# Kernel tuning notes

Hardware: AMD Instinct MI355X
Metric: run time of the kernel (lower is better)

Reference implementation:

```python
import math
import jax, jax.numpy as jnp
import numpy as np

B, T, E = 4, 2048, 768
H, D = 3, E // 3  # 3 heads, head_dim = emb_sz // 3
USE_MASK = True


def setup_inputs() -> dict:
    key = jax.random.key(0)
    ks = jax.random.split(key, 8)
    s_in = 1.0 / math.sqrt(E)
    return {
        "inputs_for_keys": jax.random.normal(ks[0], (B, T, E), jnp.float32),
        "inputs_for_values": jax.random.normal(ks[1], (B, T, E), jnp.float32),
        "inputs_for_queries": jax.random.normal(ks[2], (B, T, E), jnp.float32),
        # per-head projection weights, stacked over head axis: [H, E, D]
        "Wk": jax.random.normal(ks[3], (H, E, D), jnp.float32) * s_in,
        "Wq": jax.random.normal(ks[4], (H, E, D), jnp.float32) * s_in,
        "Wv": jax.random.normal(ks[5], (H, E, D), jnp.float32) * s_in,
        # final Dense(emb_sz)
        "Wo": jax.random.normal(ks[6], (E, E), jnp.float32) * s_in,
        "bo": jnp.zeros((E,), jnp.float32),
    }


def reference(inputs_for_keys, inputs_for_values, inputs_for_queries, Wk, Wq, Wv, Wo, bo):
    # Project per head: [B,T,E] x [H,E,D] -> [B,H,T,D]
    K = jnp.einsum('bte,hed->bhtd', inputs_for_keys, Wk)
    V = jnp.einsum('bte,hed->bhtd', inputs_for_values, Wv)
    Q = jnp.einsum('bte,hed->bhtd', inputs_for_queries, Wq)
    # NOTE: original scales by sqrt(window_size_keys) = sqrt(T), not sqrt(D)
    scores = jnp.einsum('bhqd,bhkd->bhqk', Q, K) / math.sqrt(T)
    if USE_MASK:
        mask = jnp.triu(jnp.full((T, T), -jnp.inf, dtype=scores.dtype), k=1)
        scores = scores + mask
    attn = jax.nn.softmax(scores, axis=-1)  # [B,H,Tq,Tk]
    z = jnp.einsum('bhqk,bhkd->bhqd', attn, V)  # [B,H,T,D]
    # concat heads in order head1,head2,head3 along last axis -> [B,T,E]
    z = jnp.transpose(z, (0, 2, 1, 3)).reshape(B, T, H * D)
    return z @ Wo + bo
```

## Files before the change

### kernel.cpp

```cpp
#include <hip/hip_runtime.h>
#include <hip/hip_bf16.h>
#include <math.h>

#define B_ 4
#define T_ 2048
#define E_ 768
#define H_ 3
#define D_ 256
#define LOG2E 1.4426950408889634f

typedef __attribute__((ext_vector_type(8))) _Float16 half8;
typedef __attribute__((ext_vector_type(8))) unsigned short ushort8;
typedef __attribute__((ext_vector_type(4))) float f32x4;

static __device__ inline unsigned short f2h(float x) {
    _Float16 h = (_Float16)x;
    return *reinterpret_cast<unsigned short*>(&h);
}

#define GLOAD_LDS(SRC, DST) \
    __builtin_amdgcn_global_load_lds( \
        (const __attribute__((address_space(1))) void*)(SRC), \
        (__attribute__((address_space(3))) void*)(DST), 16, 0, 0)

__global__ __launch_bounds__(256)
void transpose_cast_all(const float* __restrict__ Wk, const float* __restrict__ Wq,
                        const float* __restrict__ Wv, const float* __restrict__ Wo,
                        unsigned short* __restrict__ WTk, unsigned short* __restrict__ WTq,
                        unsigned short* __restrict__ WTv, unsigned short* __restrict__ WoT)
{
    __shared__ float tile[32][33];
    const int z = blockIdx.z;
    const float* in; unsigned short* out; int R, C;
    if (z < 9) {
        const int mat = z / 3, hd = z % 3;
        R = E_; C = D_;
        in  = (mat == 0 ? Wk  : mat == 1 ? Wq  : Wv)  + (long)hd * E_ * D_;
        out = (mat == 0 ? WTk : mat == 1 ? WTq : WTv) + (long)hd * D_ * E_;
    } else {
        R = E_; C = E_;
        in = Wo; out = WoT;
    }
    const int c0 = blockIdx.x * 32;
    const int r0 = blockIdx.y * 32;
    if (c0 >= C) return;
    const int t  = threadIdx.x;
    const int cc = t & 31, rr = t >> 5;
    #pragma unroll
    for (int i = 0; i < 4; ++i)
        tile[rr + i * 8][cc] = in[(long)(r0 + rr + i * 8) * C + c0 + cc];
    __syncthreads();
    const int rr2 = t & 31, cc2 = t >> 5;
    #pragma unroll
    for (int i = 0; i < 4; ++i)
        out[(long)(c0 + cc2 + i * 8) * R + r0 + rr2] = f2h(tile[rr2][cc2 + i * 8]);
}

template<bool CONVA, bool OUT16, bool TRANSC>
__device__ __forceinline__
void gemm_body(const float* Af, const unsigned short* Ah, const unsigned short* Bz,
               void* Cz, const float* bias, int K, int lda, int ldc,
               int m0, int n0, int tid)
{
    __shared__ unsigned short As[128 * 32];
    __shared__ unsigned short Bs[128 * 32];

    const int lane = tid & 63, wid = tid >> 6;
    const int wm = wid >> 1, wn = wid & 1;
    const int fr = lane & 15, fg = lane >> 4;

    f32x4 acc[4][4];
    #pragma unroll
    for (int mt = 0; mt < 4; ++mt)
        #pragma unroll
        for (int nt = 0; nt < 4; ++nt) acc[mt][nt] = (f32x4)(0.f);

    for (int k0 = 0; k0 < K; k0 += 32) {
        #pragma unroll
        for (int i = 0; i < 2; ++i) {
            const int G = tid + i * 256;
            const int row = G >> 2, g = G & 3;
            ushort8 pa;
            if (CONVA) {
                const float* s = Af + (long)(m0 + row) * lda + k0 + g * 8;
                float4 f0 = *(const float4*)s, f1 = *(const float4*)(s + 4);
                pa[0] = f2h(f0.x); pa[1] = f2h(f0.y); pa[2] = f2h(f0.z); pa[3] = f2h(f0.w);
                pa[4] = f2h(f1.x); pa[5] = f2h(f1.y); pa[6] = f2h(f1.z); pa[7] = f2h(f1.w);
            } else {
                pa = *(const ushort8*)(Ah + (long)(m0 + row) * lda + k0 + g * 8);
            }
            *(ushort8*)&As[row * 32 + g * 8] = pa;
            *(ushort8*)&Bs[row * 32 + g * 8] =
                *(const ushort8*)(Bz + (long)(n0 + row) * K + k0 + g * 8);
        }
        __syncthreads();

        half8 a[4], b[4];
        #pragma unroll
        for (int mt = 0; mt < 4; ++mt)
            a[mt] = *(const half8*)&As[(wm * 64 + mt * 16 + fr) * 32 + fg * 8];
        #pragma unroll
        for (int nt = 0; nt < 4; ++nt)
            b[nt] = *(const half8*)&Bs[(wn * 64 + nt * 16 + fr) * 32 + fg * 8];
        #pragma unroll
        for (int mt = 0; mt < 4; ++mt)
            #pragma unroll
            for (int nt = 0; nt < 4; ++nt)
                acc[mt][nt] = __builtin_amdgcn_mfma_f32_16x16x32_f16(
                                  a[mt], b[nt], acc[mt][nt], 0, 0, 0);
        __syncthreads();
    }

    #pragma unroll
    for (int nt = 0; nt < 4; ++nt) {
        const int col = n0 + wn * 64 + nt * 16 + fr;
        const float badd = bias ? bias[col] : 0.f;
        #pragma unroll
        for (int mt = 0; mt < 4; ++mt) {
            const int row = m0 + wm * 64 + mt * 16 + fg * 4;
            #pragma unroll
            for (int reg = 0; reg < 4; ++reg) {
                const float vv = acc[mt][nt][reg] + badd;
                if (TRANSC)
                    ((unsigned short*)Cz)[(long)col * ldc + row + reg] = f2h(vv);
                else if (OUT16)
                    ((unsigned short*)Cz)[(long)(row + reg) * ldc + col] = f2h(vv);
                else
                    ((float*)Cz)[(long)(row + reg) * ldc + col] = vv;
            }
        }
    }
}

template<bool CONVA, bool OUT16>
__global__ __launch_bounds__(256)
void gemm_mfma(const void* __restrict__ Av, const unsigned short* __restrict__ Bt,
               void* __restrict__ Cv, const float* __restrict__ bias,
               int K, int Hdiv, int lda, int ldc, long sA, long sB, long sC)
{
    const int z = blockIdx.z;
    const float*          Af = (const float*)Av          + (long)(z / Hdiv) * sA;
    const unsigned short* Ah = (const unsigned short*)Av + (long)(z / Hdiv) * sA;
    const unsigned short* Bz = Bt + (long)(z % Hdiv) * sB;
    void* Cz = OUT16 ? (void*)((unsigned short*)Cv + (long)z * sC)
                     : (void*)((float*)Cv + (long)z * sC);
    gemm_body<CONVA, OUT16, false>(Af, Ah, Bz, Cz, bias, K, lda, ldc,
                                   blockIdx.y * 128, blockIdx.x * 128, threadIdx.x);
}

__global__ __launch_bounds__(256)
void qkv_proj(const float* __restrict__ Xk, const float* __restrict__ Xv,
              const float* __restrict__ Xq,
              const unsigned short* __restrict__ WTk, const unsigned short* __restrict__ WTv,
              const unsigned short* __restrict__ WTq,
              unsigned short* __restrict__ Kp, unsigned short* __restrict__ Vt,
              unsigned short* __restrict__ Qp)
{
    const int z = blockIdx.z;
    const int which = z / 12, bh = z % 12;
    const int b = bh / H_, h = bh % H_;
    const int m0 = blockIdx.y * 128, n0 = blockIdx.x * 128;
    const int tid = threadIdx.x;
    if (which == 1) {
        const float* Af = Xv + (long)b * T_ * E_;
        const unsigned short* Bz = WTv + (long)h * D_ * E_;
        unsigned short* Cz = Vt + (long)bh * D_ * T_;
        gemm_body<true, true, true>(Af, nullptr, Bz, Cz, nullptr, E_, E_, T_, m0, n0, tid);
    } else {
        const float* X = (which == 0) ? Xk : Xq;
        const unsigned short* W = (which == 0) ? WTk : WTq;
        unsigned short* P = (which == 0) ? Kp : Qp;
        const float* Af = X + (long)b * T_ * E_;
        const unsigned short* Bz = W + (long)h * D_ * E_;
        unsigned short* Cz = P + (long)bh * T_ * D_;
        gemm_body<true, true, false>(Af, nullptr, Bz, Cz, nullptr, E_, E_, D_, m0, n0, tid);
    }
}

__global__ __launch_bounds__(512, 1)
void flash_lds(const unsigned short* __restrict__ Qb, const unsigned short* __restrict__ Kb,
               const unsigned short* __restrict__ Vtb, unsigned short* __restrict__ Z2h,
               float scale_log2e)
{
    __shared__ unsigned short Ktile[2][64 * 256];
    __shared__ unsigned short Vtile[2][256 * 64];
    __shared__ unsigned short Ps[8][16 * 72];

    const int p  = blockIdx.x;
    const int l  = (p & 7) * 24 + (p >> 3);
    const int bh = l >> 4;
    const int pi = l & 15;
    const int b = bh / H_, h = bh % H_;
    const int tid = threadIdx.x;
    const int w = tid >> 6, lane = tid & 63;
    const int g = lane >> 4, fr = lane & 15;
    const int qw0 = (w < 4) ? (pi * 64 + w * 16) : ((31 - pi) * 64 + (w - 4) * 16);

    const unsigned short* kg = Kb  + (long)bh * T_ * D_;
    const unsigned short* vg = Vtb + (long)bh * D_ * T_;

    const unsigned short* qrow = Qb + ((long)bh * T_ + qw0 + fr) * D_;
    const _Float16 hs = (_Float16)scale_log2e;
    half8 qf[8];
    #pragma unroll
    for (int c = 0; c < 8; ++c) {
        qf[c] = *(const half8*)(qrow + c * 32 + g * 8);
        qf[c] *= hs;
    }

    f32x4 o[16];
    #pragma unroll
    for (int dt = 0; dt < 16; ++dt) o[dt] = (f32x4)(0.f);
    float mrow[4] = {-INFINITY, -INFINITY, -INFINITY, -INFINITY};
    float lrow[4] = {0.f, 0.f, 0.f, 0.f};

    const int nkt = 32 - pi;

    auto STAGE = [&](int bufi, int kt) {
        const int k0 = kt * 64;
        #pragma unroll
        for (int i = 0; i < 4; ++i) {
            const int L = tid + i * 512;
            const int r = L >> 5, cg = L & 31;
            GLOAD_LDS(kg + (long)(k0 + r) * D_ + ((cg ^ (r & 7)) * 8),
                      &Ktile[bufi][L * 8]);
        }
        #pragma unroll
        for (int i = 0; i < 4; ++i) {
            const int L = tid + i * 512;
            const int dr = L >> 3, gq = L & 7;
            GLOAD_LDS(vg + (long)dr * T_ + k0 + ((gq ^ (dr & 7)) * 8),
                      &Vtile[bufi][L * 8]);
        }
    };

    STAGE(0, 0);
    int buf = 0;
    for (int kt = 0; kt < nkt; ++kt) {
        asm volatile("s_waitcnt vmcnt(0)" ::: "memory");
        __builtin_amdgcn_sched_barrier(0);
        __builtin_amdgcn_s_barrier();
        __builtin_amdgcn_sched_barrier(0);
        if (kt + 1 < nkt)
            STAGE(buf ^ 1, kt + 1);

        const int k0 = kt * 64;
        if (k0 <= qw0 + 15) {
            f32x4 s[4];
            #pragma unroll
            for (int nt = 0; nt < 4; ++nt) s[nt] = (f32x4)(0.f);
            const int kkey = fr & 7;
            __builtin_amdgcn_s_setprio(1);
            #pragma unroll
            for (int c = 0; c < 8; ++c) {
                #pragma unroll
                for (int nt = 0; nt < 4; ++nt) {
                    const int kr = nt * 16 + fr;
                    half8 kf = *(const half8*)&Ktile[buf][(kr * 32 + ((c * 4 + g) ^ kkey)) * 8];
                    s[nt] = __builtin_amdgcn_mfma_f32_16x16x32_f16(qf[c], kf, s[nt], 0, 0, 0);
                }
            }
            __builtin_amdgcn_s_setprio(0);

            const bool diag = (k0 + 63 > qw0);
            float sv[4][4];
            #pragma unroll
            for (int nt = 0; nt < 4; ++nt)
                #pragma unroll
                for (int reg = 0; reg < 4; ++reg) {
                    float v = s[nt][reg];
                    if (diag && (k0 + nt * 16 + fr > qw0 + g * 4 + reg)) v = -INFINITY;
                    sv[nt][reg] = v;
                }

            float pmax[4];
            #pragma unroll
            for (int reg = 0; reg < 4; ++reg)
                pmax[reg] = fmaxf(fmaxf(sv[0][reg], sv[1][reg]),
                                  fmaxf(sv[2][reg], sv[3][reg]));
            const bool ok = (pmax[0] <= mrow[0] + 8.f) && (pmax[1] <= mrow[1] + 8.f)
                         && (pmax[2] <= mrow[2] + 8.f) && (pmax[3] <= mrow[3] + 8.f);
            if (!__all(ok)) {
                #pragma unroll
                for (int reg = 0; reg < 4; ++reg) {
                    float tm = pmax[reg];
                    tm = fmaxf(tm, __shfl_xor(tm, 1));
                    tm = fmaxf(tm, __shfl_xor(tm, 2));
                    tm = fmaxf(tm, __shfl_xor(tm, 4));
                    tm = fmaxf(tm, __shfl_xor(tm, 8));
                    const float mnew = fmaxf(mrow[reg], tm);
                    const float alpha = exp2f(mrow[reg] - mnew);
                    mrow[reg] = mnew;
                    lrow[reg] *= alpha;
                    #pragma unroll
                    for (int dt = 0; dt < 16; ++dt) o[dt][reg] *= alpha;
                }
            }
            #pragma unroll
            for (int nt = 0; nt < 4; ++nt)
                #pragma unroll
                for (int reg = 0; reg < 4; ++reg) {
                    const float pp = exp2f(sv[nt][reg] - mrow[reg]);
                    lrow[reg] += pp;
                    Ps[w][(g * 4 + reg) * 72 + nt * 16 + fr] = f2h(pp);
                }

            const half8 pf0 = *(const half8*)&Ps[w][fr * 72 + g * 8];
            const half8 pf1 = *(const half8*)&Ps[w][fr * 72 + 32 + g * 8];

            __builtin_amdgcn_s_setprio(1);
            #pragma unroll
            for (int dt = 0; dt < 16; ++dt) {
                const int dr = dt * 16 + fr;
                const int key = dr & 7;
                half8 vf0 = *(const half8*)&Vtile[buf][(dr * 8 + (g ^ key)) * 8];
                o[dt] = __builtin_amdgcn_mfma_f32_16x16x32_f16(pf0, vf0, o[dt], 0, 0, 0);
                half8 vf1 = *(const half8*)&Vtile[buf][(dr * 8 + ((g + 4) ^ key)) * 8];
                o[dt] = __builtin_amdgcn_mfma_f32_16x16x32_f16(pf1, vf1, o[dt], 0, 0, 0);
            }
            __builtin_amdgcn_s_setprio(0);
        }
        buf ^= 1;
    }

    float inv[4];
    #pragma unroll
    for (int reg = 0; reg < 4; ++reg) {
        float ps = lrow[reg];
        ps += __shfl_xor(ps, 1);
        ps += __shfl_xor(ps, 2);
        ps += __shfl_xor(ps, 4);
        ps += __shfl_xor(ps, 8);
        inv[reg] = 1.f / ps;
    }
    const long rowbase = ((long)b * T_ + qw0 + g * 4) * E_ + h * D_;
    #pragma unroll
    for (int reg = 0; reg < 4; ++reg) {
        unsigned short* dst = Z2h + rowbase + (long)reg * E_ + fr;
        #pragma unroll
        for (int dt = 0; dt < 16; ++dt)
            dst[dt * 16] = f2h(o[dt][reg] * inv[reg]);
    }
}

extern "C" void kernel_launch(void* const* d_in, const int* in_sizes, int n_in,
                              void* d_out, int out_size, void* d_ws, size_t ws_size,
                              hipStream_t stream)
{
    const float* Xk = (const float*)d_in[0];
    const float* Xv = (const float*)d_in[1];
    const float* Xq = (const float*)d_in[2];
    const float* Wk = (const float*)d_in[3];
    const float* Wq = (const float*)d_in[4];
    const float* Wv = (const float*)d_in[5];
    const float* Wo = (const float*)d_in[6];
    const float* bo = (const float*)d_in[7];
    float* out = (float*)d_out;

    const size_t phd = (size_t)B_ * H_ * T_ * D_;
    const size_t wsz = (size_t)H_ * E_ * D_;
    unsigned short* Kp  = (unsigned short*)d_ws;
    unsigned short* Vp  = Kp + phd;
    unsigned short* Qp  = Vp + phd;
    unsigned short* Vt  = Qp + phd;
    unsigned short* Z2h = Vt + phd;
    unsigned short* WTk = Z2h + (size_t)B_ * T_ * E_;
    unsigned short* WTq = WTk + wsz;
    unsigned short* WTv = WTq + wsz;
    unsigned short* WoT = WTv + wsz;

    dim3 blk(256);

    dim3 gtw(E_ / 32, E_ / 32, 10);
    transpose_cast_all<<<gtw, blk, 0, stream>>>(Wk, Wq, Wv, Wo, WTk, WTq, WTv, WoT);

    dim3 gproj(D_ / 128, T_ / 128, 36);
    qkv_proj<<<gproj, blk, 0, stream>>>(Xk, Xv, Xq, WTk, WTv, WTq, Kp, Vt, Qp);

    dim3 gf(16 * B_ * H_);
    dim3 fblk(512);
    flash_lds<<<gf, fblk, 0, stream>>>(Qp, Kp, Vt, Z2h,
                                       0.022097086912079608f * LOG2E);

    dim3 gout(E_ / 128, (B_ * T_) / 128, 1);
    gemm_mfma<false, false><<<gout, blk, 0, stream>>>(Z2h, WoT, out, bo, E_, 1, E_, E_,
                                                      0L, 0L, 0L);
}
```

Baseline: 178.5 us.

## Use 32x32 MFMA with wave pairs splitting head dim in flash attention

```diff
diff --git a/kernel.cpp b/kernel.cpp
--- a/kernel.cpp
+++ b/kernel.cpp
@@ -12,6 +12,7 @@
 typedef __attribute__((ext_vector_type(8))) _Float16 half8;
 typedef __attribute__((ext_vector_type(8))) unsigned short ushort8;
 typedef __attribute__((ext_vector_type(4))) float f32x4;
+typedef __attribute__((ext_vector_type(16))) float f32x16;
 
 static __device__ inline unsigned short f2h(float x) {
     _Float16 h = (_Float16)x;
@@ -177,14 +178,14 @@
     }
 }
 
-__global__ __launch_bounds__(512, 1)
+__global__ __launch_bounds__(512, 2)
 void flash_lds(const unsigned short* __restrict__ Qb, const unsigned short* __restrict__ Kb,
                const unsigned short* __restrict__ Vtb, unsigned short* __restrict__ Z2h,
                float scale_log2e)
 {
     __shared__ unsigned short Ktile[2][64 * 256];
     __shared__ unsigned short Vtile[2][256 * 64];
-    __shared__ unsigned short Ps[8][16 * 72];
+    __shared__ unsigned short Ps[4][32 * 64];
 
     const int p  = blockIdx.x;
     const int l  = (p & 7) * 24 + (p >> 3);
@@ -193,26 +194,29 @@
     const int b = bh / H_, h = bh % H_;
     const int tid = threadIdx.x;
     const int w = tid >> 6, lane = tid & 63;
-    const int g = lane >> 4, fr = lane & 15;
-    const int qw0 = (w < 4) ? (pi * 64 + w * 16) : ((31 - pi) * 64 + (w - 4) * 16);
+    const int sw = w >> 1, dhalf = w & 1;
+    const int lo = lane & 31, hi = lane >> 5;
+    const int qw0 = (sw < 2) ? (pi * 64 + sw * 32)
+                             : ((31 - pi) * 64 + (sw - 2) * 32);
 
     const unsigned short* kg = Kb  + (long)bh * T_ * D_;
     const unsigned short* vg = Vtb + (long)bh * D_ * T_;
 
-    const unsigned short* qrow = Qb + ((long)bh * T_ + qw0 + fr) * D_;
+    const unsigned short* qrow = Qb + ((long)bh * T_ + qw0 + lo) * D_ + hi * 8;
     const _Float16 hs = (_Float16)scale_log2e;
-    half8 qf[8];
-    #pragma unroll
-    for (int c = 0; c < 8; ++c) {
-        qf[c] = *(const half8*)(qrow + c * 32 + g * 8);
+    half8 qf[16];
+    #pragma unroll
+    for (int c = 0; c < 16; ++c) {
+        qf[c] = *(const half8*)(qrow + c * 16);
         qf[c] *= hs;
     }
 
-    f32x4 o[16];
-    #pragma unroll
-    for (int dt = 0; dt < 16; ++dt) o[dt] = (f32x4)(0.f);
-    float mrow[4] = {-INFINITY, -INFINITY, -INFINITY, -INFINITY};
-    float lrow[4] = {0.f, 0.f, 0.f, 0.f};
+    f32x16 o[4];
+    #pragma unroll
+    for (int dt = 0; dt < 4; ++dt) o[dt] = (f32x16)(0.f);
+    float mrow[16], lrow[16];
+    #pragma unroll
+    for (int reg = 0; reg < 16; ++reg) { mrow[reg] = -INFINITY; lrow[reg] = 0.f; }
 
     const int nkt = 32 - pi;
 
@@ -245,101 +249,110 @@
             STAGE(buf ^ 1, kt + 1);
 
         const int k0 = kt * 64;
-        if (k0 <= qw0 + 15) {
-            f32x4 s[4];
-            #pragma unroll
-            for (int nt = 0; nt < 4; ++nt) s[nt] = (f32x4)(0.f);
-            const int kkey = fr & 7;
+        const bool live = (k0 <= qw0 + 31);
+        float sv0[16], sv1[16];
+        if (live) {
+            f32x16 s0 = (f32x16)(0.f), s1 = (f32x16)(0.f);
+            const int kkey = lo & 7;
             __builtin_amdgcn_s_setprio(1);
             #pragma unroll
-            for (int c = 0; c < 8; ++c) {
+            for (int c = 0; c < 16; ++c) {
+                half8 kf0 = *(const half8*)&Ktile[buf][(lo * 32 + ((c * 2 + hi) ^ kkey)) * 8];
+                s0 = __builtin_amdgcn_mfma_f32_32x32x16_f16(qf[c], kf0, s0, 0, 0, 0);
+                half8 kf1 = *(const half8*)&Ktile[buf][((32 + lo) * 32 + ((c * 2 + hi) ^ kkey)) * 8];
+                s1 = __builtin_amdgcn_mfma_f32_32x32x16_f16(qf[c], kf1, s1, 0, 0, 0);
+            }
+            __builtin_amdgcn_s_setprio(0);
+
+            const bool diag = (k0 + 63 > qw0);
+            bool okl = true;
+            #pragma unroll
+            for (int reg = 0; reg < 16; ++reg) {
+                const int row = (reg & 3) + 8 * (reg >> 2) + 4 * hi;
+                const int qa = qw0 + row;
+                float v0 = s0[reg], v1 = s1[reg];
+                if (diag && (k0 + lo > qa))      v0 = -INFINITY;
+                if (diag && (k0 + 32 + lo > qa)) v1 = -INFINITY;
+                sv0[reg] = v0; sv1[reg] = v1;
+                okl = okl && (fmaxf(v0, v1) <= mrow[reg] + 8.f);
+            }
+            if (!__all(okl)) {
                 #pragma unroll
-                for (int nt = 0; nt < 4; ++nt) {
-                    const int kr = nt * 16 + fr;
-                    half8 kf = *(const half8*)&Ktile[buf][(kr * 32 + ((c * 4 + g) ^ kkey)) * 8];
-                    s[nt] = __builtin_amdgcn_mfma_f32_16x16x32_f16(qf[c], kf, s[nt], 0, 0, 0);
-                }
-            }
-            __builtin_amdgcn_s_setprio(0);
-
-            const bool diag = (k0 + 63 > qw0);
-            float sv[4][4];
-            #pragma unroll
-            for (int nt = 0; nt < 4; ++nt)
-                #pragma unroll
-                for (int reg = 0; reg < 4; ++reg) {
-                    float v = s[nt][reg];
-                    if (diag && (k0 + nt * 16 + fr > qw0 + g * 4 + reg)) v = -INFINITY;
-                    sv[nt][reg] = v;
-                }
-
-            float pmax[4];
-            #pragma unroll
-            for (int reg = 0; reg < 4; ++reg)
-                pmax[reg] = fmaxf(fmaxf(sv[0][reg], sv[1][reg]),
-                                  fmaxf(sv[2][reg], sv[3][reg]));
-            const bool ok = (pmax[0] <= mrow[0] + 8.f) && (pmax[1] <= mrow[1] + 8.f)
-                         && (pmax[2] <= mrow[2] + 8.f) && (pmax[3] <= mrow[3] + 8.f);
-            if (!__all(ok)) {
-                #pragma unroll
-                for (int reg = 0; reg < 4; ++reg) {
-                    float tm = pmax[reg];
+                for (int reg = 0; reg < 16; ++reg) {
+                    float tm = fmaxf(sv0[reg], sv1[reg]);
                     tm = fmaxf(tm, __shfl_xor(tm, 1));
                     tm = fmaxf(tm, __shfl_xor(tm, 2));
                     tm = fmaxf(tm, __shfl_xor(tm, 4));
                     tm = fmaxf(tm, __shfl_xor(tm, 8));
+                    tm = fmaxf(tm, __shfl_xor(tm, 16));
                     const float mnew = fmaxf(mrow[reg], tm);
                     const float alpha = exp2f(mrow[reg] - mnew);
                     mrow[reg] = mnew;
                     lrow[reg] *= alpha;
                     #pragma unroll
-                    for (int dt = 0; dt < 16; ++dt) o[dt][reg] *= alpha;
+                    for (int dt = 0; dt < 4; ++dt) o[dt][reg] *= alpha;
                 }
             }
             #pragma unroll
-            for (int nt = 0; nt < 4; ++nt)
+            for (int reg = 0; reg < 16; ++reg) {
+                const int row = (reg & 3) + 8 * (reg >> 2) + 4 * hi;
+                const float pp0 = exp2f(sv0[reg] - mrow[reg]);
+                const float pp1 = exp2f(sv1[reg] - mrow[reg]);
+                lrow[reg] += pp0 + pp1;
+                if (dhalf == 0) {
+                    const int rk = row & 7;
+                    Ps[sw][row * 64 + (((lo >> 3) ^ rk) * 8) + (lo & 7)] = f2h(pp0);
+                    Ps[sw][row * 64 + ((((lo + 32) >> 3) ^ rk) * 8) + (lo & 7)] = f2h(pp1);
+                }
+            }
+        }
+
+        __builtin_amdgcn_sched_barrier(0);
+        __builtin_amdgcn_s_barrier();
+        __builtin_amdgcn_sched_barrier(0);
+
+        if (live) {
+            half8 pf[4];
+            const int pkey = lo & 7;
+            #pragma unroll
+            for (int ks = 0; ks < 4; ++ks)
+                pf[ks] = *(const half8*)&Ps[sw][lo * 64 + (((ks * 2 + hi) ^ pkey) * 8)];
+
+            __builtin_amdgcn_s_setprio(1);
+            #pragma unroll
+            for (int dt = 0; dt < 4; ++dt) {
+                const int dr = dhalf * 128 + dt * 32 + lo;
+                const int vkey = dr & 7;
                 #pragma unroll
-                for (int reg = 0; reg < 4; ++reg) {
-                    const float pp = exp2f(sv[nt][reg] - mrow[reg]);
-                    lrow[reg] += pp;
-                    Ps[w][(g * 4 + reg) * 72 + nt * 16 + fr] = f2h(pp);
+                for (int ks = 0; ks < 4; ++ks) {
+                    half8 vf = *(const half8*)&Vtile[buf][(dr * 8 + ((ks * 2 + hi) ^ vkey)) * 8];
+                    o[dt] = __builtin_amdgcn_mfma_f32_32x32x16_f16(pf[ks], vf, o[dt], 0, 0, 0);
                 }
-
-            const half8 pf0 = *(const half8*)&Ps[w][fr * 72 + g * 8];
-            const half8 pf1 = *(const half8*)&Ps[w][fr * 72 + 32 + g * 8];
-
-            __builtin_amdgcn_s_setprio(1);
-            #pragma unroll
-            for (int dt = 0; dt < 16; ++dt) {
-                const int dr = dt * 16 + fr;
-                const int key = dr & 7;
-                half8 vf0 = *(const half8*)&Vtile[buf][(dr * 8 + (g ^ key)) * 8];
-                o[dt] = __builtin_amdgcn_mfma_f32_16x16x32_f16(pf0, vf0, o[dt], 0, 0, 0);
-                half8 vf1 = *(const half8*)&Vtile[buf][(dr * 8 + ((g + 4) ^ key)) * 8];
-                o[dt] = __builtin_amdgcn_mfma_f32_16x16x32_f16(pf1, vf1, o[dt], 0, 0, 0);
             }
             __builtin_amdgcn_s_setprio(0);
         }
         buf ^= 1;
     }
 
-    float inv[4];
-    #pragma unroll
-    for (int reg = 0; reg < 4; ++reg) {
+    float inv[16];
+    #pragma unroll
+    for (int reg = 0; reg < 16; ++reg) {
         float ps = lrow[reg];
         ps += __shfl_xor(ps, 1);
         ps += __shfl_xor(ps, 2);
         ps += __shfl_xor(ps, 4);
         ps += __shfl_xor(ps, 8);
+        ps += __shfl_xor(ps, 16);
         inv[reg] = 1.f / ps;
     }
-    const long rowbase = ((long)b * T_ + qw0 + g * 4) * E_ + h * D_;
-    #pragma unroll
-    for (int reg = 0; reg < 4; ++reg) {
-        unsigned short* dst = Z2h + rowbase + (long)reg * E_ + fr;
-        #pragma unroll
-        for (int dt = 0; dt < 16; ++dt)
-            dst[dt * 16] = f2h(o[dt][reg] * inv[reg]);
+    #pragma unroll
+    for (int reg = 0; reg < 16; ++reg) {
+        const int row = (reg & 3) + 8 * (reg >> 2) + 4 * hi;
+        unsigned short* dst = Z2h + ((long)b * T_ + qw0 + row) * E_ + h * D_
+                                  + dhalf * 128 + lo;
+        #pragma unroll
+        for (int dt = 0; dt < 4; ++dt)
+            dst[dt * 32] = f2h(o[dt][reg] * inv[reg]);
     }
 }
 
```

Result: slower. 327.3 us (+83.3%).

## Double-buffer GEMM LDS tiles with direct global-to-LDS loads and prefetch

Applied to the files above, without the earlier changes.

```diff
diff --git a/kernel.cpp b/kernel.cpp
--- a/kernel.cpp
+++ b/kernel.cpp
@@ -62,53 +62,91 @@
                void* Cz, const float* bias, int K, int lda, int ldc,
                int m0, int n0, int tid)
 {
-    __shared__ unsigned short As[128 * 32];
-    __shared__ unsigned short Bs[128 * 32];
+    __shared__ unsigned short As[2][128 * 32];
+    __shared__ unsigned short Bs[2][128 * 32];
 
     const int lane = tid & 63, wid = tid >> 6;
     const int wm = wid >> 1, wn = wid & 1;
     const int fr = lane & 15, fg = lane >> 4;
-
-    f32x4 acc[4][4];
-    #pragma unroll
-    for (int mt = 0; mt < 4; ++mt)
-        #pragma unroll
-        for (int nt = 0; nt < 4; ++nt) acc[mt][nt] = (f32x4)(0.f);
-
-    for (int k0 = 0; k0 < K; k0 += 32) {
+    const int NK = K >> 5;
+
+    float4 fA[2][2];
+
+    auto ISSUE_A = [&](int bufi, int k0) {
         #pragma unroll
         for (int i = 0; i < 2; ++i) {
             const int G = tid + i * 256;
             const int row = G >> 2, g = G & 3;
-            ushort8 pa;
             if (CONVA) {
                 const float* s = Af + (long)(m0 + row) * lda + k0 + g * 8;
-                float4 f0 = *(const float4*)s, f1 = *(const float4*)(s + 4);
-                pa[0] = f2h(f0.x); pa[1] = f2h(f0.y); pa[2] = f2h(f0.z); pa[3] = f2h(f0.w);
-                pa[4] = f2h(f1.x); pa[5] = f2h(f1.y); pa[6] = f2h(f1.z); pa[7] = f2h(f1.w);
+                fA[i][0] = *(const float4*)s;
+                fA[i][1] = *(const float4*)(s + 4);
             } else {
-                pa = *(const ushort8*)(Ah + (long)(m0 + row) * lda + k0 + g * 8);
+                GLOAD_LDS(Ah + (long)(m0 + row) * lda + k0 + g * 8,
+                          &As[bufi][G * 8]);
             }
-            *(ushort8*)&As[row * 32 + g * 8] = pa;
-            *(ushort8*)&Bs[row * 32 + g * 8] =
-                *(const ushort8*)(Bz + (long)(n0 + row) * K + k0 + g * 8);
-        }
-        __syncthreads();
+        }
+    };
+    auto ISSUE_B = [&](int bufi, int k0) {
+        #pragma unroll
+        for (int i = 0; i < 2; ++i) {
+            const int G = tid + i * 256;
+            const int row = G >> 2, g = G & 3;
+            GLOAD_LDS(Bz + (long)(n0 + row) * K + k0 + g * 8,
+                      &Bs[bufi][G * 8]);
+        }
+    };
+    auto WRITE_A = [&](int bufi) {
+        #pragma unroll
+        for (int i = 0; i < 2; ++i) {
+            const int G = tid + i * 256;
+            ushort8 pa;
+            pa[0] = f2h(fA[i][0].x); pa[1] = f2h(fA[i][0].y);
+            pa[2] = f2h(fA[i][0].z); pa[3] = f2h(fA[i][0].w);
+            pa[4] = f2h(fA[i][1].x); pa[5] = f2h(fA[i][1].y);
+            pa[6] = f2h(fA[i][1].z); pa[7] = f2h(fA[i][1].w);
+            *(ushort8*)&As[bufi][G * 8] = pa;
+        }
+    };
+
+    f32x4 acc[4][4];
+    #pragma unroll
+    for (int mt = 0; mt < 4; ++mt)
+        #pragma unroll
+        for (int nt = 0; nt < 4; ++nt) acc[mt][nt] = (f32x4)(0.f);
+
+    ISSUE_A(0, 0);
+    ISSUE_B(0, 0);
+    int buf = 0;
+    for (int kt = 0; kt < NK; ++kt) {
+        asm volatile("s_waitcnt vmcnt(0)" ::: "memory");
+        __builtin_amdgcn_sched_barrier(0);
+        if (CONVA) {
+            WRITE_A(buf);
+            asm volatile("s_waitcnt lgkmcnt(0)" ::: "memory");
+            __builtin_amdgcn_sched_barrier(0);
+        }
+        __builtin_amdgcn_s_barrier();
+        __builtin_amdgcn_sched_barrier(0);
+        if (kt + 1 < NK) {
+            ISSUE_A(buf ^ 1, (kt + 1) << 5);
+            ISSUE_B(buf ^ 1, (kt + 1) << 5);
+        }
 
         half8 a[4], b[4];
         #pragma unroll
         for (int mt = 0; mt < 4; ++mt)
-            a[mt] = *(const half8*)&As[(wm * 64 + mt * 16 + fr) * 32 + fg * 8];
+            a[mt] = *(const half8*)&As[buf][(wm * 64 + mt * 16 + fr) * 32 + fg * 8];
         #pragma unroll
         for (int nt = 0; nt < 4; ++nt)
-            b[nt] = *(const half8*)&Bs[(wn * 64 + nt * 16 + fr) * 32 + fg * 8];
+            b[nt] = *(const half8*)&Bs[buf][(wn * 64 + nt * 16 + fr) * 32 + fg * 8];
         #pragma unroll
         for (int mt = 0; mt < 4; ++mt)
             #pragma unroll
             for (int nt = 0; nt < 4; ++nt)
                 acc[mt][nt] = __builtin_amdgcn_mfma_f32_16x16x32_f16(
                                   a[mt], b[nt], acc[mt][nt], 0, 0, 0);
-        __syncthreads();
+        buf ^= 1;
     }
 
     #pragma unroll
```

After: 210.2 us. +17.8%, slower.
